# Optimization experiments

Hardware: AMD Instinct MI355X
Metric: run time of the kernel (lower is better)

Reference implementation:

```python
import jax, jax.numpy as jnp
import numpy as np

B, C, H, W = 4, 256, 32, 32
DS, DC, EXP, NSL, NH = 16, 4, 2, 16, 2
DI = EXP * C
DTR = (C + 15) // 16


def layer_norm(x, w, b, eps=1e-5):
    m = x.mean(-1, keepdims=True)
    v = ((x - m) ** 2).mean(-1, keepdims=True)
    return (x - m) / jnp.sqrt(v + eps) * w + b


def conv2d(x, w, b, groups=1, pad=1):
    y = jax.lax.conv_general_dilated(x, w, (1, 1), [(pad, pad), (pad, pad)],
        dimension_numbers=('NCHW', 'OIHW', 'NCHW'), feature_group_count=groups)
    return y + b[None, :, None, None]


def causal_conv1d(x, w, b):
    k = w.shape[-1]
    y = jax.lax.conv_general_dilated(x, w, (1,), [(k - 1, 0)],
        dimension_numbers=('NCH', 'OIH', 'NCH'), feature_group_count=x.shape[1])
    return y + b[None, :, None]


def selective_scan(u, delta, A, Bm, Cm, D, z):
    # u, delta, z: (b,d,l); A: (d,n); Bm, Cm: (b,n,l); D: (d,)
    dA = jnp.exp(jnp.einsum('bdl,dn->lbdn', delta, A))
    dBu = jnp.einsum('bdl,bnl->lbdn', delta * u, Bm)
    Cl = jnp.moveaxis(Cm, -1, 0)  # (l,b,n)
    def step(s, inp):
        dA_t, dBu_t, C_t = inp
        s = dA_t * s + dBu_t
        return s, jnp.einsum('bdn,bn->bd', s, C_t)
    s0 = jnp.zeros(dA.shape[1:], dA.dtype)
    _, ys = jax.lax.scan(step, s0, (dA, dBu, Cl))
    y = jnp.moveaxis(ys, 0, -1) + D[None, :, None] * u
    return y * jax.nn.silu(z)


def mamba_inner(xz, cw, cb, xpw, dtw, dtb, A, D):
    d = xz.shape[1] // 2
    xm, z = xz[:, :d], xz[:, d:]
    xm = jax.nn.silu(causal_conv1d(xm, cw, cb))
    x_dbl = jnp.einsum('bdl,ed->ble', xm, xpw)  # e = dt_rank + 2*d_state
    dt = x_dbl[..., :DTR]
    Bm = x_dbl[..., DTR:DTR + DS]
    Cm = x_dbl[..., DTR + DS:]
    dt = jax.nn.softplus(jnp.einsum('blr,dr->bdl', dt, dtw) + dtb[None, :, None])
    return selective_scan(xm, dt, A, jnp.moveaxis(Bm, -1, 1), jnp.moveaxis(Cm, -1, 1), D, z)


def mamba_v3(hs, in_w, cw, cb, cbw, cbb, csw, csb, xpw, xpbw, xpsw,
             dtw, dtb, dtbw, dtbb, dtsw, dtsb, Alog, Ablog, Aslog, D, Db, Ds, outw):
    b, l, dm = hs.shape
    xz = jnp.einsum('bld,ed->bel', hs, in_w)  # (b, 2*DI, l)
    A, A_b, A_s = -jnp.exp(Alog), -jnp.exp(Ablog), -jnp.exp(Aslog)
    out = mamba_inner(xz, cw, cb, xpw, dtw, dtb, A, D)
    out_b = mamba_inner(xz[:, :, ::-1], cbw, cbb, xpbw, dtbw, dtbb, A_b, Db)
    # slice scan: torch.chunk(nslices,-1) -> stack(-1) -> flatten(-2)
    xz_s = xz.reshape(b, 2 * DI, NSL, l // NSL).transpose(0, 1, 3, 2).reshape(b, 2 * DI, l)
    out_s = mamba_inner(xz_s, csw, csb, xpsw, dtsw, dtsb, A_s, Ds)
    # restore: reshape(b,d,nslices,l//nslices).permute(0,1,3,2).flatten(-2)
    out_s = out_s.reshape(b, DI, NSL, l // NSL).transpose(0, 1, 3, 2).reshape(b, DI, l)
    comb = out + out_b[:, :, ::-1] + out_s
    return jnp.einsum('bdl,od->blo', comb, outw)


def forward(x, proj1_w, proj1_b, proj2_w, proj2_b, norm_w, norm_b,
            q_w, q_b, k_w, k_b, v_w, v_b, o_w, o_b, fc1_w, fc1_b, dw_w, dw_b,
            in_w, cw, cb, cbw, cbb, csw, csb, xpw, xpbw, xpsw,
            dtw, dtb, dtbw, dtbb, dtsw, dtsb, Alog, Ablog, Aslog, D, Db, Ds, outw):
    b, c, h, w = x.shape
    n = h * w
    x_skip = x
    # torch: x.transpose(1,2).reshape(B,C,H,W) -- memory reinterpret, replicated
    x_flat = jnp.transpose(x, (0, 2, 1, 3)).reshape(b, c, h, w)
    xc = conv2d(x_flat, proj1_w, proj1_b)
    xc = jnp.transpose(xc.reshape(b, c, n), (0, 2, 1))
    xc = layer_norm(xc, norm_w, norm_b)
    dh = c // NH
    Q = (xc @ q_w.T + q_b).reshape(b, n, NH, dh).transpose(0, 2, 1, 3)
    K = (xc @ k_w.T + k_b).reshape(b, n, NH, dh).transpose(0, 2, 1, 3)
    V = (xc @ v_w.T + v_b).reshape(b, n, NH, dh).transpose(0, 2, 1, 3)
    scores = jnp.einsum('bhqd,bhkd->bhqk', Q, K) / jnp.sqrt(jnp.float32(dh))
    probs = jax.nn.softmax(scores, axis=-1)
    att = jnp.einsum('bhqk,bhkd->bhqd', probs, V).transpose(0, 2, 1, 3).reshape(b, n, c)
    att = att @ o_w.T + o_b
    # torch: .view(B,C,HW).transpose(1,2) -- memory reinterpret, replicated
    x_att = jnp.transpose(att.reshape(b, c, n), (0, 2, 1))
    xm = mamba_v3(x_att, in_w, cw, cb, cbw, cbb, csw, csb, xpw, xpbw, xpsw,
                  dtw, dtb, dtbw, dtbb, dtsw, dtsb, Alog, Ablog, Aslog, D, Db, Ds, outw)
    xm = jnp.transpose(xm, (0, 2, 1)).reshape(b, c, h, w)
    xm = jax.nn.relu(conv2d(xm, proj1_w, proj1_b))  # proj1 reused (as in source)
    xm = jax.nn.relu(conv2d(xm, proj2_w, proj2_b, pad=0))
    xs = jnp.transpose(xm.reshape(b, c, n), (0, 2, 1))
    xf = xs @ fc1_w.T + fc1_b
    xd = jnp.transpose(xf, (0, 2, 1)).reshape(b, c, h, w)
    xd = conv2d(xd, dw_w, dw_b, groups=c)
    xd = jnp.transpose(xd.reshape(b, c, n), (0, 2, 1))
    out = jnp.transpose(xd.reshape(b, h, w, c), (0, 3, 1, 2)) + x_skip
    return out


def setup_inputs():
    keys = iter(jax.random.split(jax.random.key(0), 64))
    def rn(shape, s=0.02):
        return jax.random.normal(next(keys), shape, jnp.float32) * s
    Alog = jnp.log(jnp.tile(jnp.arange(1, DS + 1, dtype=jnp.float32), (DI, 1)))
    return dict(
        x=jax.random.normal(next(keys), (B, C, H, W), jnp.float32),
        proj1_w=rn((C, C, 3, 3)), proj1_b=jnp.zeros((C,), jnp.float32),
        proj2_w=rn((C, C, 1, 1)), proj2_b=jnp.zeros((C,), jnp.float32),
        norm_w=jnp.ones((C,), jnp.float32), norm_b=jnp.zeros((C,), jnp.float32),
        q_w=rn((C, C)), q_b=jnp.zeros((C,), jnp.float32),
        k_w=rn((C, C)), k_b=jnp.zeros((C,), jnp.float32),
        v_w=rn((C, C)), v_b=jnp.zeros((C,), jnp.float32),
        o_w=rn((C, C)), o_b=jnp.zeros((C,), jnp.float32),
        fc1_w=rn((C, C)), fc1_b=jnp.zeros((C,), jnp.float32),
        dw_w=rn((C, 1, 3, 3)), dw_b=jnp.zeros((C,), jnp.float32),
        in_w=rn((2 * DI, C)),
        cw=rn((DI, 1, DC), 0.1), cb=jnp.zeros((DI,), jnp.float32),
        cbw=rn((DI, 1, DC), 0.1), cbb=jnp.zeros((DI,), jnp.float32),
        csw=rn((DI, 1, DC), 0.1), csb=jnp.zeros((DI,), jnp.float32),
        xpw=rn((DTR + 2 * DS, DI)), xpbw=rn((DTR + 2 * DS, DI)), xpsw=rn((DTR + 2 * DS, DI)),
        dtw=rn((DI, DTR), 0.1), dtb=jnp.full((DI,), -4.6, jnp.float32),
        dtbw=rn((DI, DTR), 0.1), dtbb=jnp.full((DI,), -4.6, jnp.float32),
        dtsw=rn((DI, DTR), 0.1), dtsb=jnp.full((DI,), -4.6, jnp.float32),
        Alog=Alog, Ablog=Alog, Aslog=Alog,
        D=jnp.ones((DI,), jnp.float32), Db=jnp.ones((DI,), jnp.float32), Ds=jnp.ones((DI,), jnp.float32),
        outw=rn((C, DI)),
    )


def reference(x, proj1_w, proj1_b, proj2_w, proj2_b, norm_w, norm_b,
              q_w, q_b, k_w, k_b, v_w, v_b, o_w, o_b, fc1_w, fc1_b, dw_w, dw_b,
              in_w, cw, cb, cbw, cbb, csw, csb, xpw, xpbw, xpsw,
              dtw, dtb, dtbw, dtbb, dtsw, dtsb, Alog, Ablog, Aslog, D, Db, Ds, outw):
    return forward(x, proj1_w, proj1_b, proj2_w, proj2_b, norm_w, norm_b,
                   q_w, q_b, k_w, k_b, v_w, v_b, o_w, o_b, fc1_w, fc1_b, dw_w, dw_b,
                   in_w, cw, cb, cbw, cbb, csw, csb, xpw, xpbw, xpsw,
                   dtw, dtb, dtbw, dtbb, dtsw, dtsb, Alog, Ablog, Aslog, D, Db, Ds, outw)
```

## Files before the change

### kernel.cpp

```cpp
#include <hip/hip_runtime.h>


#define LOG2E 1.4426950408889634f
#define NCH 16
#define LCH 64

typedef unsigned short u16;
typedef unsigned int u32;
typedef __attribute__((ext_vector_type(8))) short bf16x8;
typedef __attribute__((ext_vector_type(4))) float f32x4;

__device__ __forceinline__ u16 f2b(float f) {
  u32 u = __builtin_bit_cast(u32, f);
  u32 r = (u + 0x7fffu + ((u >> 16) & 1u)) >> 16;
  return (u16)r;
}
__device__ __forceinline__ float b2f(u16 h) {
  u32 u = ((u32)h) << 16;
  return __builtin_bit_cast(float, u);
}

#define DPP_ADD(p, ctrl)                                                   \
  (p) += __builtin_bit_cast(float, __builtin_amdgcn_update_dpp(            \
             0, __builtin_bit_cast(int, (p)), ctrl, 0xF, 0xF, true))

static const long BRS = 44544;

__global__ __launch_bounds__(256) void pack_branch_k(
    float* __restrict__ dst, const float* __restrict__ cw,
    const float* __restrict__ cb, const float* __restrict__ xpw,
    const float* __restrict__ dtw, const float* __restrict__ dtb,
    const float* __restrict__ Alog, const float* __restrict__ Dv) {
  int t = blockIdx.x * 256 + threadIdx.x;
  if (t < 2048) dst[t] = cw[t];
  else if (t < 2560) dst[t] = cb[t - 2048];
  else if (t < 27136) dst[t] = xpw[t - 2560];
  else if (t < 35328) dst[t] = dtw[t - 27136];
  else if (t < 35840) dst[t] = dtb[t - 35328];
  else if (t < 44032) dst[t] = -expf(Alog[t - 35840]) * LOG2E;
  else if (t < 44544) dst[t] = Dv[t - 44032];
}

__global__ __launch_bounds__(256) void pack_wb_k(
    const float* __restrict__ qw, const float* __restrict__ kw,
    const float* __restrict__ vw, const float* __restrict__ ow,
    const float* __restrict__ inw, const float* __restrict__ outw,
    const float* __restrict__ p2w, const float* __restrict__ fc1w,
    const float* __restrict__ qb, const float* __restrict__ kb,
    const float* __restrict__ vb, u16* __restrict__ WB,
    float* __restrict__ QBIAS) {
  int t = blockIdx.x * 256 + threadIdx.x;
  if (t < 65536) WB[t] = f2b(qw[t]);
  else if (t < 131072) WB[t] = f2b(kw[t - 65536]);
  else if (t < 196608) WB[t] = f2b(vw[t - 131072]);
  else if (t < 262144) WB[t] = f2b(ow[t - 196608]);
  else if (t < 524288) WB[t] = f2b(inw[t - 262144]);
  else if (t < 655360) WB[t] = f2b(outw[t - 524288]);
  else if (t < 720896) WB[t] = f2b(p2w[t - 655360]);
  else if (t < 786432) WB[t] = f2b(fc1w[t - 720896]);
  else if (t < 787200) {
    int i = t - 786432;
    QBIAS[i] = (i < 256) ? qb[i] : (i < 512 ? kb[i - 256] : vb[i - 512]);
  }
}

__global__ __launch_bounds__(256) void pack_wc_k(const float* __restrict__ w,
                                                 u16* __restrict__ wc) {
  int t = blockIdx.x * 256 + threadIdx.x;
  int ci = t & 255, khw = (t >> 8) % 9, co = t / 2304;
  wc[t] = f2b(w[co * 2304 + ci * 9 + khw]);
}

__global__ __launch_bounds__(256) void xin_k(const float* __restrict__ x,
                                             u16* __restrict__ xin) {
  int t = blockIdx.x * 256 + threadIdx.x;
  int ci = t & 255, w = (t >> 8) & 31, h = (t >> 13) & 31, b = t >> 18;
  int idx = ci * 32 + h;
  xin[t] = f2b(x[((long)b << 18) + ((long)(idx & 255) << 10) +
                 ((idx >> 8) << 5) + w]);
}

__global__ __launch_bounds__(256, 2) void conv_mfma_k(
    const u16* __restrict__ in, const u16* __restrict__ wc,
    const float* __restrict__ bias, float* __restrict__ outF,
    u16* __restrict__ outH, int relu) {
  __shared__ u16 ldsA[4][64][8];
  __shared__ u16 ldsB[4][64][8];
  int m0 = blockIdx.x * 64, n0 = blockIdx.y * 64;
  int tid = threadIdx.x;
  int lane = tid & 63, wv = tid >> 6;
  int row = tid & 63, k8 = tid >> 6;
  int l = m0 + row;
  int h = (l >> 5) & 31, w = l & 31;
  int rlo = lane & 15, khl = lane >> 4;
  f32x4 acc[4];
  #pragma unroll
  for (int n = 0; n < 4; ++n) acc[n] = (f32x4){0.f, 0.f, 0.f, 0.f};
  for (int t = 0; t < 72; ++t) {
    int kh = t / 24, r = t % 24, kw = r >> 3, ci0 = (r & 7) << 5;
    __syncthreads();
    bf16x8 av = (bf16x8){0, 0, 0, 0, 0, 0, 0, 0};
    int hh = h + kh - 1, ww = w + kw - 1;
    if ((unsigned)hh < 32u && (unsigned)ww < 32u)
      av = *(const bf16x8*)&in[(long)(l + (kh - 1) * 32 + (kw - 1)) * 256 +
                               ci0 + k8 * 8];
    *(bf16x8*)&ldsA[k8][row][0] = av;
    *(bf16x8*)&ldsB[k8][row][0] =
        *(const bf16x8*)&wc[(long)(n0 + row) * 2304 + t * 32 + k8 * 8];
    __syncthreads();
    bf16x8 af = *(const bf16x8*)&ldsA[khl][wv * 16 + rlo][0];
    #pragma unroll
    for (int n = 0; n < 4; ++n) {
      bf16x8 bf = *(const bf16x8*)&ldsB[khl][n * 16 + rlo][0];
      acc[n] = __builtin_amdgcn_mfma_f32_16x16x32_bf16(af, bf, acc[n], 0, 0, 0);
    }
  }
  int rowb = (lane >> 4) * 4;
  #pragma unroll
  for (int n = 0; n < 4; ++n) {
    int gn = n0 + n * 16 + rlo;
    float bv = bias[gn];
    #pragma unroll
    for (int j = 0; j < 4; ++j) {
      int gm = m0 + wv * 16 + rowb + j;
      float v = acc[n][j] + bv;
      if (relu) v = fmaxf(v, 0.f);
      long oi = (long)gm * 256 + gn;
      if (outH) outH[oi] = f2b(v);
      else outF[oi] = v;
    }
  }
}

__global__ __launch_bounds__(256) void layernorm_k(const float* __restrict__ x,
                                                   const float* __restrict__ w,
                                                   const float* __restrict__ b,
                                                   u16* __restrict__ o) {
  int row = blockIdx.x * 4 + (threadIdx.x >> 6);
  int lane = threadIdx.x & 63;
  float4 v = ((const float4*)(x + (long)row * 256))[lane];
  float s = v.x + v.y + v.z + v.w;
  #pragma unroll
  for (int m = 32; m; m >>= 1) s += __shfl_xor(s, m);
  float mean = s * (1.f / 256.f);
  float4 dv = {v.x - mean, v.y - mean, v.z - mean, v.w - mean};
  float vs = dv.x * dv.x + dv.y * dv.y + dv.z * dv.z + dv.w * dv.w;
  #pragma unroll
  for (int m = 32; m; m >>= 1) vs += __shfl_xor(vs, m);
  float inv = rsqrtf(vs * (1.f / 256.f) + 1e-5f);
  float4 wv = ((const float4*)w)[lane];
  float4 bv = ((const float4*)b)[lane];
  u32 lo = (u32)f2b(dv.x * inv * wv.x + bv.x) |
           ((u32)f2b(dv.y * inv * wv.y + bv.y) << 16);
  u32 hi = (u32)f2b(dv.z * inv * wv.z + bv.z) |
           ((u32)f2b(dv.w * inv * wv.w + bv.w) << 16);
  ((uint2*)(o + (long)row * 256))[lane] = make_uint2(lo, hi);
}

__global__ __launch_bounds__(256) void softmax_k(const float* __restrict__ S,
                                                 u16* __restrict__ P) {
  int row = blockIdx.x * 4 + (threadIdx.x >> 6);
  int lane = threadIdx.x & 63;
  const float4* p = (const float4*)(S + (long)row * 1024);
  float4 v[4];
  float m = -1e30f;
  #pragma unroll
  for (int i = 0; i < 4; ++i) {
    v[i] = p[lane * 4 + i];
    m = fmaxf(m, fmaxf(fmaxf(v[i].x, v[i].y), fmaxf(v[i].z, v[i].w)));
  }
  #pragma unroll
  for (int q = 32; q; q >>= 1) m = fmaxf(m, __shfl_xor(m, q));
  float s = 0.f;
  #pragma unroll
  for (int i = 0; i < 4; ++i) {
    v[i].x = expf(v[i].x - m); v[i].y = expf(v[i].y - m);
    v[i].z = expf(v[i].z - m); v[i].w = expf(v[i].w - m);
    s += v[i].x + v[i].y + v[i].z + v[i].w;
  }
  #pragma unroll
  for (int q = 32; q; q >>= 1) s += __shfl_xor(s, q);
  float inv = 1.f / s;
  uint2* q2 = (uint2*)(P + (long)row * 1024);
  #pragma unroll
  for (int i = 0; i < 4; ++i) {
    u32 lo = (u32)f2b(v[i].x * inv) | ((u32)f2b(v[i].y * inv) << 16);
    u32 hi = (u32)f2b(v[i].z * inv) | ((u32)f2b(v[i].w * inv) << 16);
    q2[lane * 4 + i] = make_uint2(lo, hi);
  }
}

__global__ __launch_bounds__(256, 2) void bgemm_k(
    const u16* __restrict__ A, const u16* __restrict__ B,
    const float* __restrict__ bias, float* __restrict__ OutF,
    u16* __restrict__ OutH, int M, int N, int K,
    int lda, int ldb, int ldo, int zdiv,
    long a_zb, long a_zh, long b_zb, long b_zh, long o_zb, long o_zh,
    float alpha, int act) {
  __shared__ u16 ldsA[4][128][8];
  __shared__ u16 ldsB[4][128][8];
  int z = blockIdx.z, zb = z / zdiv, zh = z - zb * zdiv;
  const u16* Ab = A + zb * a_zb + zh * a_zh;
  const u16* Bb = B + zb * b_zb + zh * b_zh;
  long ob = zb * o_zb + zh * o_zh;
  int m0 = blockIdx.x * 128, n0 = blockIdx.y * 128;
  int tid = threadIdx.x;
  int lane = tid & 63, wv = tid >> 6;
  int wr = wv >> 1, wc = wv & 1;
  int r1 = tid & 127, h1 = tid >> 7;
  int r2 = r1, h2 = h1 + 2;
  const u16* a1 = Ab + (long)(m0 + r1) * lda + h1 * 8;
  const u16* a2 = Ab + (long)(m0 + r2) * lda + h2 * 8;
  const u16* b1 = Bb + (long)(n0 + r1) * ldb + h1 * 8;
  const u16* b2 = Bb + (long)(n0 + r2) * ldb + h2 * 8;

  f32x4 acc[4][4];
  #pragma unroll
  for (int i = 0; i < 4; ++i)
    #pragma unroll
    for (int j = 0; j < 4; ++j) acc[i][j] = (f32x4){0.f, 0.f, 0.f, 0.f};

  bf16x8 ra1 = *(const bf16x8*)a1;
  bf16x8 ra2 = *(const bf16x8*)a2;
  bf16x8 rb1 = *(const bf16x8*)b1;
  bf16x8 rb2 = *(const bf16x8*)b2;

  int nt = K >> 5;
  int kh = lane >> 4, rlo = lane & 15;
  for (int t = 0; t < nt; ++t) {
    __syncthreads();
    *(bf16x8*)&ldsA[h1][r1][0] = ra1;
    *(bf16x8*)&ldsA[h2][r2][0] = ra2;
    *(bf16x8*)&ldsB[h1][r1][0] = rb1;
    *(bf16x8*)&ldsB[h2][r2][0] = rb2;
    if (t + 1 < nt) {
      int ko = (t + 1) << 5;
      ra1 = *(const bf16x8*)(a1 + ko);
      ra2 = *(const bf16x8*)(a2 + ko);
      rb1 = *(const bf16x8*)(b1 + ko);
      rb2 = *(const bf16x8*)(b2 + ko);
    }
    __syncthreads();
    bf16x8 af[4], bfr[4];
    #pragma unroll
    for (int m = 0; m < 4; ++m)
      af[m] = *(const bf16x8*)&ldsA[kh][wr * 64 + m * 16 + rlo][0];
    #pragma unroll
    for (int n = 0; n < 4; ++n)
      bfr[n] = *(const bf16x8*)&ldsB[kh][wc * 64 + n * 16 + rlo][0];
    #pragma unroll
    for (int m = 0; m < 4; ++m)
      #pragma unroll
      for (int n = 0; n < 4; ++n)
        acc[m][n] = __builtin_amdgcn_mfma_f32_16x16x32_bf16(af[m], bfr[n],
                                                            acc[m][n], 0, 0, 0);
  }
  int rowb = (lane >> 4) * 4;
  #pragma unroll
  for (int m = 0; m < 4; ++m) {
    #pragma unroll
    for (int n = 0; n < 4; ++n) {
      int gn = n0 + wc * 64 + n * 16 + rlo;
      float bv = bias ? bias[gn] : 0.f;
      #pragma unroll
      for (int j = 0; j < 4; ++j) {
        int gm = m0 + wr * 64 + m * 16 + rowb + j;
        float v = acc[m][n][j] * alpha + bv;
        if (act == 1) v = fmaxf(v, 0.f);
        long oi = ob + (long)gm * ldo + gn;
        if (OutH) OutH[oi] = f2b(v);
        else OutF[oi] = v;
      }
    }
  }
}

__global__ __launch_bounds__(256) void vt_k(const u16* __restrict__ qkv,
                                            u16* __restrict__ vt) {
  int t = blockIdx.x * 256 + threadIdx.x;
  int j = t & 1023, d = (t >> 10) & 127, bh = t >> 17;
  int b = bh >> 1, h = bh & 1;
  vt[t] = qkv[((long)(b * 1024 + j)) * 768 + 512 + h * 128 + d];
}

__global__ __launch_bounds__(256) void xatt_k(const float* __restrict__ hs,
                                              u16* __restrict__ xa) {
  int t = blockIdx.x * 256 + threadIdx.x;
  int dm = t & 255, l = (t >> 8) & 1023, b = t >> 18;
  xa[t] = f2b(hs[((long)b << 18) + dm * 1024 + l]);
}

__device__ __forceinline__ int brmap(int br, int j) {
  if (br == 0) return j;
  if (br == 1) return 1023 - j;
  return ((j & 15) << 6) | (j >> 4);
}

__global__ __launch_bounds__(256) void cconv_k(const float* __restrict__ xz,
                                               const float* __restrict__ pk,
                                               float* __restrict__ xmc,
                                               u16* __restrict__ zs) {
  long t = (long)blockIdx.x * 256 + threadIdx.x;
  int d = (int)(t & 511);
  long r = t >> 9;
  int j = (int)(r & 1023);
  int bb = (int)(r >> 10);
  int b = bb & 3, br = bb >> 2;
  const float* pb = pk + (long)br * BRS;
  float acc = pb[2048 + d];
  #pragma unroll
  for (int tap = 0; tap < 4; ++tap) {
    int jj = j - 3 + tap;
    if (jj >= 0) {
      int l = brmap(br, jj);
      acc = fmaf(xz[(((long)b << 10) + l) * 1024 + d], pb[d * 4 + tap], acc);
    }
  }
  float sig = 1.f / (1.f + expf(-acc));
  xmc[t] = acc * sig;
  int l = brmap(br, j);
  float zv = xz[(((long)b << 10) + l) * 1024 + 512 + d];
  zs[t] = f2b(zv / (1.f + expf(-zv)));
}

__global__ __launch_bounds__(256) void gemm_k(
    const float* __restrict__ A, const float* __restrict__ B,
    const float* __restrict__ bias, float* __restrict__ Out,
    int M, int N, int K,
    int a_sm, int a_sk, int b_sn, int b_sk, int o_sm,
    int zdiv, long a_zb, long a_zh, long b_zb, long b_zh, long o_zb, long o_zh,
    long bias_zb, float alpha, int act, const float* __restrict__ Aux) {
  int z = blockIdx.z, zb = z / zdiv, zh = z % zdiv;
  const float* Ab = A + zb * a_zb + zh * a_zh;
  const float* Bb = B + zb * b_zb + zh * b_zh;
  const float* biasb = bias ? (bias + zb * bias_zb) : nullptr;
  long oo = zb * o_zb + zh * o_zh;
  __shared__ float As[16][68];
  __shared__ float Bs[16][68];
  int m0 = blockIdx.x * 64, n0 = blockIdx.y * 64;
  int tid = threadIdx.x;
  int tm = tid >> 4, tn = tid & 15;
  float acc[4][4] = {};
  for (int k0 = 0; k0 < K; k0 += 16) {
    #pragma unroll
    for (int it = 0; it < 4; ++it) {
      int i = tid + it * 256;
      if (a_sk == 1) {
        int rr = i >> 4, kk = i & 15;
        int gm = m0 + rr, gk = k0 + kk;
        float av = 0.f;
        if (gm < M && gk < K) av = Ab[(long)gm * a_sm + gk];
        As[kk][rr] = av;
      } else {
        int rr = i & 63, kk = i >> 6;
        int gm = m0 + rr, gk = k0 + kk;
        float av = 0.f;
        if (gm < M && gk < K) av = Ab[(long)gm * a_sm + (long)gk * a_sk];
        As[kk][rr] = av;
      }
      if (b_sk == 1) {
        int rr = i >> 4, kk = i & 15;
        int gn = n0 + rr, gk = k0 + kk;
        float bv = 0.f;
        if (gn < N && gk < K) bv = Bb[(long)gn * b_sn + gk];
        Bs[kk][rr] = bv;
      } else {
        int rr = i & 63, kk = i >> 6;
        int gn = n0 + rr, gk = k0 + kk;
        float bv = 0.f;
        if (gn < N && gk < K) bv = Bb[(long)gn * b_sn + (long)gk * b_sk];
        Bs[kk][rr] = bv;
      }
    }
    __syncthreads();
    #pragma unroll
    for (int kk = 0; kk < 16; ++kk) {
      float ar[4], br_[4];
      #pragma unroll
      for (int q = 0; q < 4; ++q) ar[q] = As[kk][tm * 4 + q];
      #pragma unroll
      for (int q = 0; q < 4; ++q) br_[q] = Bs[kk][tn * 4 + q];
      #pragma unroll
      for (int qi = 0; qi < 4; ++qi)
        #pragma unroll
        for (int qj = 0; qj < 4; ++qj)
          acc[qi][qj] = fmaf(ar[qi], br_[qj], acc[qi][qj]);
    }
    __syncthreads();
  }
  #pragma unroll
  for (int qi = 0; qi < 4; ++qi) {
    int gm = m0 + tm * 4 + qi;
    if (gm >= M) continue;
    #pragma unroll
    for (int qj = 0; qj < 4; ++qj) {
      int gn = n0 + tn * 4 + qj;
      if (gn >= N) continue;
      float v = acc[qi][qj] * alpha + (biasb ? biasb[gn] : 0.f);
      long oid = oo + (long)gm * o_sm + gn;
      if (act == 3) {
        float sp = (v > 30.f) ? v : log1pf(expf(v));
        ((float2*)Out)[oid] = make_float2(sp, Aux[oid]);
      } else {
        if (act == 1) v = fmaxf(v, 0.f);
        else if (act == 2) v = (v > 30.f) ? v : log1pf(expf(v));
        Out[oid] = v;
      }
    }
  }
}


__global__ __launch_bounds__(256) void scanA_k(
    const float2* __restrict__ du, const float* __restrict__ xdbl,
    const float* __restrict__ pk, float* __restrict__ SE,
    float* __restrict__ PC) {
  __shared__ float bs[LCH][16];
  int tid = threadIdx.x;
  int wv = tid >> 6, lane = tid & 63;
  int q = lane & 3, dl = lane >> 2;
  int bb = blockIdx.x >> 3, dch = blockIdx.x & 7;
  int br = bb >> 2, b = bb & 3;
  int d = dch * 64 + wv * 16 + dl;
  int c = blockIdx.y;
  long xdb = (long)br * 196608 + (long)b * 49152 + (long)(c * LCH) * 48;
  {
    int j = tid >> 2, g = tid & 3;
    *(float4*)&bs[j][g * 4] = *(const float4*)&xdbl[xdb + j * 48 + 16 + g * 4];
  }
  __syncthreads();
  const float* pb = pk + (long)br * BRS;
  float4 Aln = *(const float4*)&pb[35840 + d * 16 + q * 4];
  long obase = ((long)bb << 19) + (long)(c * LCH) * 512 + d;
  const float2* pdu = du + obase;
  float4 s = {0.f, 0.f, 0.f, 0.f};
  float S = 0.f;
  #pragma unroll 4
  for (int jl = 0; jl < LCH; ++jl) {
    float2 dv = pdu[(long)jl * 512];
    float w = dv.x * dv.y;
    float4 Bv = *(const float4*)&bs[jl][q * 4];
    s.x = fmaf(exp2f(dv.x * Aln.x), s.x, w * Bv.x);
    s.y = fmaf(exp2f(dv.x * Aln.y), s.y, w * Bv.y);
    s.z = fmaf(exp2f(dv.x * Aln.z), s.z, w * Bv.z);
    s.w = fmaf(exp2f(dv.x * Aln.w), s.w, w * Bv.w);
    S += dv.x;
  }
  long si = ((((long)bb) * NCH + c) * 512 + d) * 16 + q * 4;
  *(float4*)&SE[si] = s;
  float4 P = {exp2f(Aln.x * S), exp2f(Aln.y * S),
              exp2f(Aln.z * S), exp2f(Aln.w * S)};
  *(float4*)&PC[si] = P;
}

__global__ __launch_bounds__(256) void scanB_k(const float* __restrict__ SE,
                                               const float* __restrict__ PC,
                                               float* __restrict__ SI) {
  long t = (long)blockIdx.x * 256 + threadIdx.x;
  int n = (int)(t & 15);
  int d = (int)((t >> 4) & 511);
  int bb = (int)(t >> 13);
  float run = 0.f;
  for (int c = 0; c < NCH; ++c) {
    long si = (((long)bb * NCH + c) * 512 + d) * 16 + n;
    SI[si] = run;
    run = fmaf(PC[si], run, SE[si]);
  }
}

__global__ __launch_bounds__(256) void scanC_k(
    const float2* __restrict__ du, const float* __restrict__ xdbl,
    const u16* __restrict__ zs, const float* __restrict__ pk,
    const float* __restrict__ SI, u16* __restrict__ y) {
  __shared__ float bcs[LCH][32];
  int tid = threadIdx.x;
  int wv = tid >> 6, lane = tid & 63;
  int q = lane & 3, dl = lane >> 2;
  int bb = blockIdx.x >> 3, dch = blockIdx.x & 7;
  int br = bb >> 2, b = bb & 3;
  int d = dch * 64 + wv * 16 + dl;
  int c = blockIdx.y;
  long xdb = (long)br * 196608 + (long)b * 49152 + (long)(c * LCH) * 48;
  #pragma unroll
  for (int i = 0; i < 2; ++i) {
    int idx = tid + i * 256;
    int j = idx >> 3, g = idx & 7;
    *(float4*)&bcs[j][g * 4] = *(const float4*)&xdbl[xdb + j * 48 + 16 + g * 4];
  }
  __syncthreads();
  const float* pb = pk + (long)br * BRS;
  float4 Aln = *(const float4*)&pb[35840 + d * 16 + q * 4];
  float Dv = pb[44032 + d];
  long obase = ((long)bb << 19) + (long)(c * LCH) * 512 + d;
  long si = ((((long)bb) * NCH + c) * 512 + d) * 16 + q * 4;
  float4 s = *(const float4*)&SI[si];
  const float2* pdu = du + obase;
  const u16* pzs = zs + obase;
  u16* py = y + obase;
  #pragma unroll 4
  for (int jl = 0; jl < LCH; ++jl) {
    float2 dv = pdu[(long)jl * 512];
    float w = dv.x * dv.y;
    float4 Bv = *(const float4*)&bcs[jl][q * 4];
    float4 Cv = *(const float4*)&bcs[jl][16 + q * 4];
    s.x = fmaf(exp2f(dv.x * Aln.x), s.x, w * Bv.x);
    s.y = fmaf(exp2f(dv.x * Aln.y), s.y, w * Bv.y);
    s.z = fmaf(exp2f(dv.x * Aln.z), s.z, w * Bv.z);
    s.w = fmaf(exp2f(dv.x * Aln.w), s.w, w * Bv.w);
    float p = s.x * Cv.x;
    p = fmaf(s.y, Cv.y, p);
    p = fmaf(s.z, Cv.z, p);
    p = fmaf(s.w, Cv.w, p);
    DPP_ADD(p, 0xB1);
    DPP_ADD(p, 0x4E);
    if (q == 0)
      py[(long)jl * 512] = f2b((p + Dv * dv.y) * b2f(pzs[(long)jl * 512]));
  }
}

__global__ __launch_bounds__(256) void combine_k(const u16* __restrict__ y,
                                                 u16* __restrict__ comb) {
  long t = (long)blockIdx.x * 256 + threadIdx.x;
  int d = (int)(t & 511);
  long r = t >> 9;
  int l = (int)(r & 1023);
  int b = (int)(r >> 10);
  int j2 = ((l & 63) << 4) | (l >> 6);
  float v = b2f(y[(((long)b << 10) + l) * 512 + d])
          + b2f(y[(((long)(4 + b) << 10) + (1023 - l)) * 512 + d])
          + b2f(y[(((long)(8 + b) << 10) + j2) * 512 + d]);
  comb[t] = f2b(v);
}

__global__ __launch_bounds__(256) void dw_k(const float* __restrict__ xf,
                                            const float* __restrict__ dww,
                                            const float* __restrict__ dwb,
                                            const float* __restrict__ x,
                                            float* __restrict__ out) {
  int t = blockIdx.x;
  int b = t >> 5, h = t & 31;
  int c = threadIdx.x;
  float wv[9];
  #pragma unroll
  for (int k = 0; k < 9; ++k) wv[k] = dww[c * 9 + k];
  float bb = dwb[c];
  for (int w = 0; w < 32; ++w) {
    float acc = bb;
    #pragma unroll
    for (int kh = 0; kh < 3; ++kh) {
      int hh = h + kh - 1;
      if ((unsigned)hh >= 32u) continue;
      #pragma unroll
      for (int kw = 0; kw < 3; ++kw) {
        int ww = w + kw - 1;
        if ((unsigned)ww >= 32u) continue;
        acc = fmaf(xf[(((long)b << 10) + (hh << 5) + ww) * 256 + c],
                   wv[kh * 3 + kw], acc);
      }
    }
    long oi = (((long)b * 256 + c) * 32 + h) * 32 + w;
    out[oi] = acc + x[oi];
  }
}

extern "C" void kernel_launch(void* const* d_in, const int* in_sizes, int n_in,
                              void* d_out, int out_size, void* d_ws, size_t ws_size,
                              hipStream_t stream) {
  (void)in_sizes; (void)n_in; (void)out_size; (void)ws_size;
  const float* x    = (const float*)d_in[0];
  const float* p1w  = (const float*)d_in[1];
  const float* p1b  = (const float*)d_in[2];
  const float* p2w  = (const float*)d_in[3];
  const float* p2b  = (const float*)d_in[4];
  const float* nw   = (const float*)d_in[5];
  const float* nb   = (const float*)d_in[6];
  const float* qw   = (const float*)d_in[7];
  const float* qb   = (const float*)d_in[8];
  const float* kw   = (const float*)d_in[9];
  const float* kb   = (const float*)d_in[10];
  const float* vw   = (const float*)d_in[11];
  const float* vb   = (const float*)d_in[12];
  const float* ow   = (const float*)d_in[13];
  const float* ob   = (const float*)d_in[14];
  const float* fc1w = (const float*)d_in[15];
  const float* fc1b = (const float*)d_in[16];
  const float* dww  = (const float*)d_in[17];
  const float* dwb  = (const float*)d_in[18];
  const float* inw  = (const float*)d_in[19];
  const float* cw   = (const float*)d_in[20];
  const float* cb   = (const float*)d_in[21];
  const float* cbw  = (const float*)d_in[22];
  const float* cbb  = (const float*)d_in[23];
  const float* csw  = (const float*)d_in[24];
  const float* csb  = (const float*)d_in[25];
  const float* xpw  = (const float*)d_in[26];
  const float* xpbw = (const float*)d_in[27];
  const float* xpsw = (const float*)d_in[28];
  const float* dtw  = (const float*)d_in[29];
  const float* dtb  = (const float*)d_in[30];
  const float* dtbw = (const float*)d_in[31];
  const float* dtbb = (const float*)d_in[32];
  const float* dtsw = (const float*)d_in[33];
  const float* dtsb = (const float*)d_in[34];
  const float* Alog = (const float*)d_in[35];
  const float* Ablog= (const float*)d_in[36];
  const float* Aslog= (const float*)d_in[37];
  const float* Dv   = (const float*)d_in[38];
  const float* Dbv  = (const float*)d_in[39];
  const float* Dsv  = (const float*)d_in[40];
  const float* outw = (const float*)d_in[41];
  float* out = (float*)d_out;

  float* ws    = (float*)d_ws;
  float* PB    = ws;
  u16*   WCONV = (u16*)(ws + 140000);
  u16*   WB    = (u16*)(ws + 440000);
  float* QBIAS = ws + 840000;
  u16*   XINB  = (u16*)(ws + 850000);
  float* R     = ws + 1400000;
  float*  XZ   = R;
  float2* DU   = (float2*)R;
  float*  XMC  = R + 12700000;
  u16*    Y    = (u16*)(R + 12700000);
  float*  SE   = R + 14300000;
  float*  PC   = R + 15900000;
  float*  SI   = R + 17500000;
  u16*   COMBB = (u16*)(R + 17500000);
  u16*    ZS   = (u16*)(R + 19100000);
  float*  XDBL = R + 25400000;
  float* XCT   = R + 4300000;
  u16*   XCTB  = (u16*)(R + 5400000);
  u16*   QKVB  = (u16*)(R + 6000000);
  u16*   VT    = (u16*)(R + 7600000);
  float* SC    = R + 8200000;
  u16*   P     = (u16*)(R + 16600000);
  u16*   ATTB  = (u16*)(R + 18800000);
  float* HS    = R + 19400000;
  u16*   XATTB = (u16*)(R + 20500000);
  u16*   XMBB  = (u16*)R;
  u16*   XM2B  = (u16*)(R + 600000);
  u16*   XPB   = (u16*)(R + 1200000);
  float* XF    = R + 1800000;

  u16* WQKVB = WB;
  u16* OWB   = WB + 196608;
  u16* INWB  = WB + 262144;
  u16* OUTWB = WB + 524288;
  u16* P2WB  = WB + 655360;
  u16* FC1WB = WB + 720896;

  auto bgemm = [&](const u16* A, const u16* Bm, const float* bias,
                   float* OutF, u16* OutH, int M, int N, int K,
                   int lda, int ldb, int ldo, int nz, int zdiv,
                   long a_zb, long a_zh, long b_zb, long b_zh,
                   long o_zb, long o_zh, float alpha, int act) {
    dim3 g(M / 128, N / 128, nz);
    bgemm_k<<<g, 256, 0, stream>>>(A, Bm, bias, OutF, OutH, M, N, K,
                                   lda, ldb, ldo, zdiv, a_zb, a_zh,
                                   b_zb, b_zh, o_zb, o_zh, alpha, act);
  };

  pack_branch_k<<<174, 256, 0, stream>>>(PB, cw, cb, xpw, dtw, dtb, Alog, Dv);
  pack_branch_k<<<174, 256, 0, stream>>>(PB + BRS, cbw, cbb, xpbw, dtbw, dtbb, Ablog, Dbv);
  pack_branch_k<<<174, 256, 0, stream>>>(PB + 2 * BRS, csw, csb, xpsw, dtsw, dtsb, Aslog, Dsv);
  pack_wb_k<<<3075, 256, 0, stream>>>(qw, kw, vw, ow, inw, outw, p2w, fc1w,
                                      qb, kb, vb, WB, QBIAS);
  pack_wc_k<<<2304, 256, 0, stream>>>(p1w, WCONV);
  xin_k<<<4096, 256, 0, stream>>>(x, XINB);

  conv_mfma_k<<<dim3(64, 4), 256, 0, stream>>>(XINB, WCONV, p1b, XCT, nullptr, 0);
  layernorm_k<<<1024, 256, 0, stream>>>(XCT, nw, nb, XCTB);

  bgemm(XCTB, WQKVB, QBIAS, nullptr, QKVB, 4096, 768, 256, 256, 256, 768,
        1, 1, 0, 0, 0, 0, 0, 0, 1.f, 0);
  vt_k<<<4096, 256, 0, stream>>>(QKVB, VT);

  bgemm(QKVB, QKVB + 256, nullptr, SC, nullptr, 1024, 1024, 128, 768, 768, 1024,
        8, 2, 786432, 128, 786432, 128, 2097152, 1048576,
        0.08838834764831845f, 0);
  softmax_k<<<2048, 256, 0, stream>>>(SC, P);

  bgemm(P, VT, nullptr, nullptr, ATTB, 1024, 128, 1024, 1024, 1024, 256,
        8, 2, 2097152, 1048576, 262144, 131072, 262144, 128, 1.f, 0);

  bgemm(ATTB, OWB, ob, HS, nullptr, 4096, 256, 256, 256, 256, 256,
        1, 1, 0, 0, 0, 0, 0, 0, 1.f, 0);
  xatt_k<<<4096, 256, 0, stream>>>(HS, XATTB);

  bgemm(XATTB, INWB, nullptr, XZ, nullptr, 1024, 1024, 256, 256, 256, 1024,
        4, 1, 262144, 0, 0, 0, 1048576, 0, 1.f, 0);

  cconv_k<<<24576, 256, 0, stream>>>(XZ, PB, XMC, ZS);

  {
    dim3 g(64, 1, 3);
    gemm_k<<<g, 256, 0, stream>>>(XMC, PB + 2560, nullptr, XDBL, 4096, 48, 512,
                                  512, 1, 512, 1, 48, 1, 2097152, 0, BRS, 0,
                                  196608, 0, 0, 1.f, 0, nullptr);
  }
  {
    dim3 g(64, 8, 3);
    gemm_k<<<g, 256, 0, stream>>>(XDBL, PB + 27136, PB + 35328, (float*)DU,
                                  4096, 512, 16, 48, 1, 16, 1, 512, 1,
                                  196608, 0, BRS, 0, 2097152, 0, BRS,
                                  1.f, 3, XMC);
  }

  scanA_k<<<dim3(96, NCH), 256, 0, stream>>>(DU, XDBL, PB, SE, PC);
  scanB_k<<<384, 256, 0, stream>>>(SE, PC, SI);
  scanC_k<<<dim3(96, NCH), 256, 0, stream>>>(DU, XDBL, ZS, PB, SI, Y);

  combine_k<<<8192, 256, 0, stream>>>(Y, COMBB);

  bgemm(COMBB, OUTWB, nullptr, nullptr, XMBB, 4096, 256, 512, 512, 512, 256,
        1, 1, 0, 0, 0, 0, 0, 0, 1.f, 0);

  conv_mfma_k<<<dim3(64, 4), 256, 0, stream>>>(XMBB, WCONV, p1b, nullptr, XM2B, 1);

  bgemm(XM2B, P2WB, p2b, nullptr, XPB, 4096, 256, 256, 256, 256, 256,
        1, 1, 0, 0, 0, 0, 0, 0, 1.f, 1);

  bgemm(XPB, FC1WB, fc1b, XF, nullptr, 4096, 256, 256, 256, 256, 256,
        1, 1, 0, 0, 0, 0, 0, 0, 1.f, 0);

  dw_k<<<128, 256, 0, stream>>>(XF, dww, dwb, x, out);
}
```

Before: 659.1 us.

## Fold dt projection into x_proj weights and run fused bf16 MFMA GEMM

Precomposes dt_proj with the dt rows of x_proj into one weight matrix, so a single bf16 MFMA GEMM (N=640, padded) produces B/C and the softplus delta directly. This replaces the two fp32 scalar gemm_k launches, with a new epilogue mode that writes B/C to a compact buffer and packs delta with u. The in_proj and fc1 outputs become bf16, which halves their traffic. dw_k is rewritten to stage each channel plane in LDS with coalesced output writes, and the three branch-pack launches are merged into one. The cost is lower precision for the delta path and the xz and fc1 intermediates, plus extra weight-packing kernels and wasted padded columns in the fused GEMM.

Measured after the change: 672.0 us. About the same (+2.0%).

```diff
diff --git a/kernel.cpp b/kernel.cpp
--- a/kernel.cpp
+++ b/kernel.cpp
@@ -26,19 +26,21 @@
 
 static const long BRS = 44544;
 
-__global__ __launch_bounds__(256) void pack_branch_k(
-    float* __restrict__ dst, const float* __restrict__ cw,
-    const float* __restrict__ cb, const float* __restrict__ xpw,
-    const float* __restrict__ dtw, const float* __restrict__ dtb,
-    const float* __restrict__ Alog, const float* __restrict__ Dv) {
+struct BrP { const float *cw, *cb, *xpw, *dtw, *dtb, *Al, *Dv; };
+
+__global__ __launch_bounds__(256) void pack_branch_k(float* __restrict__ dst0,
+                                                     BrP p0, BrP p1, BrP p2) {
+  int z = blockIdx.y;
+  BrP p = (z == 0) ? p0 : ((z == 1) ? p1 : p2);
+  float* dst = dst0 + (long)z * BRS;
   int t = blockIdx.x * 256 + threadIdx.x;
-  if (t < 2048) dst[t] = cw[t];
-  else if (t < 2560) dst[t] = cb[t - 2048];
-  else if (t < 27136) dst[t] = xpw[t - 2560];
-  else if (t < 35328) dst[t] = dtw[t - 27136];
-  else if (t < 35840) dst[t] = dtb[t - 35328];
-  else if (t < 44032) dst[t] = -expf(Alog[t - 35840]) * LOG2E;
-  else if (t < 44544) dst[t] = Dv[t - 44032];
+  if (t < 2048) dst[t] = p.cw[t];
+  else if (t < 2560) dst[t] = p.cb[t - 2048];
+  else if (t < 27136) dst[t] = p.xpw[t - 2560];
+  else if (t < 35328) dst[t] = p.dtw[t - 27136];
+  else if (t < 35840) dst[t] = p.dtb[t - 35328];
+  else if (t < 44032) dst[t] = -expf(p.Al[t - 35840]) * LOG2E;
+  else if (t < 44544) dst[t] = p.Dv[t - 44032];
 }
 
 __global__ __launch_bounds__(256) void pack_wb_k(
@@ -80,6 +82,44 @@
                  ((idx >> 8) << 5) + w]);
 }
 
+__global__ __launch_bounds__(256) void pack_wmb_k(const float* __restrict__ PB,
+                                                  u16* __restrict__ WMB,
+                                                  float* __restrict__ BIA) {
+  int z = blockIdx.y;
+  int t = blockIdx.x * 256 + threadIdx.x;
+  const float* pb = PB + (long)z * BRS;
+  if (t < 16384) {
+    int r = t >> 9, k = t & 511;
+    WMB[((long)z * 640 + r) * 512 + k] = f2b(pb[2560 + (16 + r) * 512 + k]);
+  } else if (t < 65536) {
+    int i = t - 16384;
+    int r = 544 + (i >> 9), k = i & 511;
+    WMB[((long)z * 640 + r) * 512 + k] = 0;
+  } else if (t < 66176) {
+    int i = t - 65536;
+    float v = 0.f;
+    if (i >= 32 && i < 544) v = pb[35328 + (i - 32)];
+    BIA[(long)z * 640 + i] = v;
+  }
+}
+
+__global__ __launch_bounds__(256) void pack_wdt_k(const float* __restrict__ PB,
+                                                  u16* __restrict__ WMB) {
+  int z = blockIdx.y, d = blockIdx.x;
+  const float* pb = PB + (long)z * BRS;
+  float dtwv[16];
+  #pragma unroll
+  for (int r = 0; r < 16; ++r) dtwv[r] = pb[27136 + d * 16 + r];
+  #pragma unroll
+  for (int i = 0; i < 2; ++i) {
+    int k = threadIdx.x + i * 256;
+    float acc = 0.f;
+    #pragma unroll
+    for (int r = 0; r < 16; ++r) acc = fmaf(dtwv[r], pb[2560 + r * 512 + k], acc);
+    WMB[((long)z * 640 + 32 + d) * 512 + k] = f2b(acc);
+  }
+}
+
 __global__ __launch_bounds__(256, 2) void conv_mfma_k(
     const u16* __restrict__ in, const u16* __restrict__ wc,
     const float* __restrict__ bias, float* __restrict__ outF,
@@ -196,12 +236,14 @@
     u16* __restrict__ OutH, int M, int N, int K,
     int lda, int ldb, int ldo, int zdiv,
     long a_zb, long a_zh, long b_zb, long b_zh, long o_zb, long o_zh,
-    float alpha, int act) {
+    float alpha, int act, int bias_zb, float* __restrict__ Out2,
+    const float* __restrict__ Aux) {
   __shared__ u16 ldsA[4][128][8];
   __shared__ u16 ldsB[4][128][8];
   int z = blockIdx.z, zb = z / zdiv, zh = z - zb * zdiv;
   const u16* Ab = A + zb * a_zb + zh * a_zh;
   const u16* Bb = B + zb * b_zb + zh * b_zh;
+  const float* biasb = bias ? bias + (long)zb * bias_zb : nullptr;
   long ob = zb * o_zb + zh * o_zh;
   int m0 = blockIdx.x * 128, n0 = blockIdx.y * 128;
   int tid = threadIdx.x;
@@ -261,15 +303,25 @@
     #pragma unroll
     for (int n = 0; n < 4; ++n) {
       int gn = n0 + wc * 64 + n * 16 + rlo;
-      float bv = bias ? bias[gn] : 0.f;
+      float bv = biasb ? biasb[gn] : 0.f;
       #pragma unroll
       for (int j = 0; j < 4; ++j) {
         int gm = m0 + wr * 64 + m * 16 + rowb + j;
         float v = acc[m][n][j] * alpha + bv;
-        if (act == 1) v = fmaxf(v, 0.f);
-        long oi = ob + (long)gm * ldo + gn;
-        if (OutH) OutH[oi] = f2b(v);
-        else OutF[oi] = v;
+        if (act == 4) {
+          if (gn < 32) {
+            Out2[(long)(zb * 4096 + gm) * 32 + gn] = v;
+          } else if (gn < 544) {
+            float sp = (v > 30.f) ? v : log1pf(expf(v));
+            long di = (long)(zb * 4096 + gm) * 512 + (gn - 32);
+            ((float2*)OutF)[di] = make_float2(sp, Aux[di]);
+          }
+        } else {
+          if (act == 1) v = fmaxf(v, 0.f);
+          long oi = ob + (long)gm * ldo + gn;
+          if (OutH) OutH[oi] = f2b(v);
+          else OutF[oi] = v;
+        }
       }
     }
   }
@@ -296,9 +348,10 @@
   return ((j & 15) << 6) | (j >> 4);
 }
 
-__global__ __launch_bounds__(256) void cconv_k(const float* __restrict__ xz,
+__global__ __launch_bounds__(256) void cconv_k(const u16* __restrict__ xzb,
                                                const float* __restrict__ pk,
                                                float* __restrict__ xmc,
+                                               u16* __restrict__ xmcb,
                                                u16* __restrict__ zs) {
   long t = (long)blockIdx.x * 256 + threadIdx.x;
   int d = (int)(t & 511);
@@ -313,103 +366,18 @@
     int jj = j - 3 + tap;
     if (jj >= 0) {
       int l = brmap(br, jj);
-      acc = fmaf(xz[(((long)b << 10) + l) * 1024 + d], pb[d * 4 + tap], acc);
+      acc = fmaf(b2f(xzb[(((long)b << 10) + l) * 1024 + d]), pb[d * 4 + tap],
+                 acc);
     }
   }
   float sig = 1.f / (1.f + expf(-acc));
-  xmc[t] = acc * sig;
+  float u = acc * sig;
+  xmc[t] = u;
+  xmcb[t] = f2b(u);
   int l = brmap(br, j);
-  float zv = xz[(((long)b << 10) + l) * 1024 + 512 + d];
+  float zv = b2f(xzb[(((long)b << 10) + l) * 1024 + 512 + d]);
   zs[t] = f2b(zv / (1.f + expf(-zv)));
 }
-
-__global__ __launch_bounds__(256) void gemm_k(
-    const float* __restrict__ A, const float* __restrict__ B,
-    const float* __restrict__ bias, float* __restrict__ Out,
-    int M, int N, int K,
-    int a_sm, int a_sk, int b_sn, int b_sk, int o_sm,
-    int zdiv, long a_zb, long a_zh, long b_zb, long b_zh, long o_zb, long o_zh,
-    long bias_zb, float alpha, int act, const float* __restrict__ Aux) {
-  int z = blockIdx.z, zb = z / zdiv, zh = z % zdiv;
-  const float* Ab = A + zb * a_zb + zh * a_zh;
-  const float* Bb = B + zb * b_zb + zh * b_zh;
-  const float* biasb = bias ? (bias + zb * bias_zb) : nullptr;
-  long oo = zb * o_zb + zh * o_zh;
-  __shared__ float As[16][68];
-  __shared__ float Bs[16][68];
-  int m0 = blockIdx.x * 64, n0 = blockIdx.y * 64;
-  int tid = threadIdx.x;
-  int tm = tid >> 4, tn = tid & 15;
-  float acc[4][4] = {};
-  for (int k0 = 0; k0 < K; k0 += 16) {
-    #pragma unroll
-    for (int it = 0; it < 4; ++it) {
-      int i = tid + it * 256;
-      if (a_sk == 1) {
-        int rr = i >> 4, kk = i & 15;
-        int gm = m0 + rr, gk = k0 + kk;
-        float av = 0.f;
-        if (gm < M && gk < K) av = Ab[(long)gm * a_sm + gk];
-        As[kk][rr] = av;
-      } else {
-        int rr = i & 63, kk = i >> 6;
-        int gm = m0 + rr, gk = k0 + kk;
-        float av = 0.f;
-        if (gm < M && gk < K) av = Ab[(long)gm * a_sm + (long)gk * a_sk];
-        As[kk][rr] = av;
-      }
-      if (b_sk == 1) {
-        int rr = i >> 4, kk = i & 15;
-        int gn = n0 + rr, gk = k0 + kk;
-        float bv = 0.f;
-        if (gn < N && gk < K) bv = Bb[(long)gn * b_sn + gk];
-        Bs[kk][rr] = bv;
-      } else {
-        int rr = i & 63, kk = i >> 6;
-        int gn = n0 + rr, gk = k0 + kk;
-        float bv = 0.f;
-        if (gn < N && gk < K) bv = Bb[(long)gn * b_sn + (long)gk * b_sk];
-        Bs[kk][rr] = bv;
-      }
-    }
-    __syncthreads();
-    #pragma unroll
-    for (int kk = 0; kk < 16; ++kk) {
-      float ar[4], br_[4];
-      #pragma unroll
-      for (int q = 0; q < 4; ++q) ar[q] = As[kk][tm * 4 + q];
-      #pragma unroll
-      for (int q = 0; q < 4; ++q) br_[q] = Bs[kk][tn * 4 + q];
-      #pragma unroll
-      for (int qi = 0; qi < 4; ++qi)
-        #pragma unroll
-        for (int qj = 0; qj < 4; ++qj)
-          acc[qi][qj] = fmaf(ar[qi], br_[qj], acc[qi][qj]);
-    }
-    __syncthreads();
-  }
-  #pragma unroll
-  for (int qi = 0; qi < 4; ++qi) {
-    int gm = m0 + tm * 4 + qi;
-    if (gm >= M) continue;
-    #pragma unroll
-    for (int qj = 0; qj < 4; ++qj) {
-      int gn = n0 + tn * 4 + qj;
-      if (gn >= N) continue;
-      float v = acc[qi][qj] * alpha + (biasb ? biasb[gn] : 0.f);
-      long oid = oo + (long)gm * o_sm + gn;
-      if (act == 3) {
-        float sp = (v > 30.f) ? v : log1pf(expf(v));
-        ((float2*)Out)[oid] = make_float2(sp, Aux[oid]);
-      } else {
-        if (act == 1) v = fmaxf(v, 0.f);
-        else if (act == 2) v = (v > 30.f) ? v : log1pf(expf(v));
-        Out[oid] = v;
-      }
-    }
-  }
-}
-
 
 __global__ __launch_bounds__(256) void scanA_k(
     const float2* __restrict__ du, const float* __restrict__ xdbl,
@@ -423,10 +391,10 @@
   int br = bb >> 2, b = bb & 3;
   int d = dch * 64 + wv * 16 + dl;
   int c = blockIdx.y;
-  long xdb = (long)br * 196608 + (long)b * 49152 + (long)(c * LCH) * 48;
+  long xdb = (long)br * 131072 + (long)b * 32768 + (long)(c * LCH) * 32;
   {
     int j = tid >> 2, g = tid & 3;
-    *(float4*)&bs[j][g * 4] = *(const float4*)&xdbl[xdb + j * 48 + 16 + g * 4];
+    *(float4*)&bs[j][g * 4] = *(const float4*)&xdbl[xdb + j * 32 + g * 4];
   }
   __syncthreads();
   const float* pb = pk + (long)br * BRS;
@@ -480,12 +448,12 @@
   int br = bb >> 2, b = bb & 3;
   int d = dch * 64 + wv * 16 + dl;
   int c = blockIdx.y;
-  long xdb = (long)br * 196608 + (long)b * 49152 + (long)(c * LCH) * 48;
+  long xdb = (long)br * 131072 + (long)b * 32768 + (long)(c * LCH) * 32;
   #pragma unroll
   for (int i = 0; i < 2; ++i) {
     int idx = tid + i * 256;
     int j = idx >> 3, g = idx & 7;
-    *(float4*)&bcs[j][g * 4] = *(const float4*)&xdbl[xdb + j * 48 + 16 + g * 4];
+    *(float4*)&bcs[j][g * 4] = *(const float4*)&xdbl[xdb + j * 32 + g * 4];
   }
   __syncthreads();
   const float* pb = pk + (long)br * BRS;
@@ -532,19 +500,30 @@
   comb[t] = f2b(v);
 }
 
-__global__ __launch_bounds__(256) void dw_k(const float* __restrict__ xf,
+__global__ __launch_bounds__(256) void dw_k(const u16* __restrict__ xfb,
                                             const float* __restrict__ dww,
                                             const float* __restrict__ dwb,
                                             const float* __restrict__ x,
                                             float* __restrict__ out) {
-  int t = blockIdx.x;
-  int b = t >> 5, h = t & 31;
-  int c = threadIdx.x;
+  __shared__ float plane[1024];
+  int bc = blockIdx.x;
+  int b = bc >> 8, c = bc & 255;
+  int tid = threadIdx.x;
+  #pragma unroll
+  for (int i = 0; i < 4; ++i) {
+    int n = tid + i * 256;
+    plane[n] = b2f(xfb[(((long)b << 10) + n) * 256 + c]);
+  }
+  __syncthreads();
   float wv[9];
   #pragma unroll
   for (int k = 0; k < 9; ++k) wv[k] = dww[c * 9 + k];
   float bb = dwb[c];
-  for (int w = 0; w < 32; ++w) {
+  long obase = ((long)(b * 256 + c)) << 10;
+  #pragma unroll
+  for (int i = 0; i < 4; ++i) {
+    int n = tid + i * 256;
+    int h = n >> 5, w = n & 31;
     float acc = bb;
     #pragma unroll
     for (int kh = 0; kh < 3; ++kh) {
@@ -554,12 +533,10 @@
       for (int kw = 0; kw < 3; ++kw) {
         int ww = w + kw - 1;
         if ((unsigned)ww >= 32u) continue;
-        acc = fmaf(xf[(((long)b << 10) + (hh << 5) + ww) * 256 + c],
-                   wv[kh * 3 + kw], acc);
+        acc = fmaf(plane[hh * 32 + ww], wv[kh * 3 + kw], acc);
       }
     }
-    long oi = (((long)b * 256 + c) * 32 + h) * 32 + w;
-    out[oi] = acc + x[oi];
+    out[obase + n] = acc + x[obase + n];
   }
 }
 
@@ -618,29 +595,33 @@
   float* QBIAS = ws + 840000;
   u16*   XINB  = (u16*)(ws + 850000);
   float* R     = ws + 1400000;
-  float*  XZ   = R;
+
+  u16*    XZB  = (u16*)R;
   float2* DU   = (float2*)R;
-  float*  XMC  = R + 12700000;
-  u16*    Y    = (u16*)(R + 12700000);
-  float*  SE   = R + 14300000;
-  float*  PC   = R + 15900000;
-  float*  SI   = R + 17500000;
-  u16*   COMBB = (u16*)(R + 17500000);
-  u16*    ZS   = (u16*)(R + 19100000);
-  float*  XDBL = R + 25400000;
+  u16*    ZS   = (u16*)(R + 12600000);
+  float*  XMC  = R + 15750000;
+  float*  SE   = R + 15750000;
+  float*  PC   = R + 17350000;
+  float*  SI   = R + 19000000;
+  u16*    Y    = (u16*)(R + 20600000);
+  u16*    XMCB = (u16*)(R + 22050000);
+  u16*   COMBB = (u16*)(R + 23750000);
+  float*  XDBL = R + 25200000;
+  u16*    WMB  = (u16*)(R + 25600000);
+  float*  BIA  = R + 26100000;
   float* XCT   = R + 4300000;
   u16*   XCTB  = (u16*)(R + 5400000);
   u16*   QKVB  = (u16*)(R + 6000000);
   u16*   VT    = (u16*)(R + 7600000);
   float* SC    = R + 8200000;
   u16*   P     = (u16*)(R + 16600000);
-  u16*   ATTB  = (u16*)(R + 18800000);
-  float* HS    = R + 19400000;
-  u16*   XATTB = (u16*)(R + 20500000);
+  u16*   ATTB  = (u16*)(R + 20900000);
+  float* HS    = R + 21500000;
+  u16*   XATTB = (u16*)(R + 22600000);
   u16*   XMBB  = (u16*)R;
   u16*   XM2B  = (u16*)(R + 600000);
   u16*   XPB   = (u16*)(R + 1200000);
-  float* XF    = R + 1800000;
+  u16*   XFB   = (u16*)(R + 1800000);
 
   u16* WQKVB = WB;
   u16* OWB   = WB + 196608;
@@ -653,58 +634,53 @@
                    float* OutF, u16* OutH, int M, int N, int K,
                    int lda, int ldb, int ldo, int nz, int zdiv,
                    long a_zb, long a_zh, long b_zb, long b_zh,
-                   long o_zb, long o_zh, float alpha, int act) {
+                   long o_zb, long o_zh, float alpha, int act,
+                   int bias_zb, float* Out2, const float* Aux) {
     dim3 g(M / 128, N / 128, nz);
     bgemm_k<<<g, 256, 0, stream>>>(A, Bm, bias, OutF, OutH, M, N, K,
                                    lda, ldb, ldo, zdiv, a_zb, a_zh,
-                                   b_zb, b_zh, o_zb, o_zh, alpha, act);
+                                   b_zb, b_zh, o_zb, o_zh, alpha, act,
+                                   bias_zb, Out2, Aux);
   };
 
-  pack_branch_k<<<174, 256, 0, stream>>>(PB, cw, cb, xpw, dtw, dtb, Alog, Dv);
-  pack_branch_k<<<174, 256, 0, stream>>>(PB + BRS, cbw, cbb, xpbw, dtbw, dtbb, Ablog, Dbv);
-  pack_branch_k<<<174, 256, 0, stream>>>(PB + 2 * BRS, csw, csb, xpsw, dtsw, dtsb, Aslog, Dsv);
+  BrP b0 = {cw, cb, xpw, dtw, dtb, Alog, Dv};
+  BrP b1 = {cbw, cbb, xpbw, dtbw, dtbb, Ablog, Dbv};
+  BrP b2 = {csw, csb, xpsw, dtsw, dtsb, Aslog, Dsv};
+  pack_branch_k<<<dim3(174, 3), 256, 0, stream>>>(PB, b0, b1, b2);
   pack_wb_k<<<3075, 256, 0, stream>>>(qw, kw, vw, ow, inw, outw, p2w, fc1w,
                                       qb, kb, vb, WB, QBIAS);
   pack_wc_k<<<2304, 256, 0, stream>>>(p1w, WCONV);
   xin_k<<<4096, 256, 0, stream>>>(x, XINB);
+  pack_wmb_k<<<dim3(259, 3), 256, 0, stream>>>(PB, WMB, BIA);
+  pack_wdt_k<<<dim3(512, 3), 256, 0, stream>>>(PB, WMB);
 
   conv_mfma_k<<<dim3(64, 4), 256, 0, stream>>>(XINB, WCONV, p1b, XCT, nullptr, 0);
   layernorm_k<<<1024, 256, 0, stream>>>(XCT, nw, nb, XCTB);
 
   bgemm(XCTB, WQKVB, QBIAS, nullptr, QKVB, 4096, 768, 256, 256, 256, 768,
-        1, 1, 0, 0, 0, 0, 0, 0, 1.f, 0);
+        1, 1, 0, 0, 0, 0, 0, 0, 1.f, 0, 0, nullptr, nullptr);
   vt_k<<<4096, 256, 0, stream>>>(QKVB, VT);
 
   bgemm(QKVB, QKVB + 256, nullptr, SC, nullptr, 1024, 1024, 128, 768, 768, 1024,
         8, 2, 786432, 128, 786432, 128, 2097152, 1048576,
-        0.08838834764831845f, 0);
+        0.08838834764831845f, 0, 0, nullptr, nullptr);
   softmax_k<<<2048, 256, 0, stream>>>(SC, P);
 
   bgemm(P, VT, nullptr, nullptr, ATTB, 1024, 128, 1024, 1024, 1024, 256,
-        8, 2, 2097152, 1048576, 262144, 131072, 262144, 128, 1.f, 0);
+        8, 2, 2097152, 1048576, 262144, 131072, 262144, 128, 1.f, 0,
+        0, nullptr, nullptr);
 
   bgemm(ATTB, OWB, ob, HS, nullptr, 4096, 256, 256, 256, 256, 256,
-        1, 1, 0, 0, 0, 0, 0, 0, 1.f, 0);
+        1, 1, 0, 0, 0, 0, 0, 0, 1.f, 0, 0, nullptr, nullptr);
   xatt_k<<<4096, 256, 0, stream>>>(HS, XATTB);
 
-  bgemm(XATTB, INWB, nullptr, XZ, nullptr, 1024, 1024, 256, 256, 256, 1024,
-        4, 1, 262144, 0, 0, 0, 1048576, 0, 1.f, 0);
-
-  cconv_k<<<24576, 256, 0, stream>>>(XZ, PB, XMC, ZS);
-
-  {
-    dim3 g(64, 1, 3);
-    gemm_k<<<g, 256, 0, stream>>>(XMC, PB + 2560, nullptr, XDBL, 4096, 48, 512,
-                                  512, 1, 512, 1, 48, 1, 2097152, 0, BRS, 0,
-                                  196608, 0, 0, 1.f, 0, nullptr);
-  }
-  {
-    dim3 g(64, 8, 3);
-    gemm_k<<<g, 256, 0, stream>>>(XDBL, PB + 27136, PB + 35328, (float*)DU,
-                                  4096, 512, 16, 48, 1, 16, 1, 512, 1,
-                                  196608, 0, BRS, 0, 2097152, 0, BRS,
-                                  1.f, 3, XMC);
-  }
+  bgemm(XATTB, INWB, nullptr, nullptr, XZB, 1024, 1024, 256, 256, 256, 1024,
+        4, 1, 262144, 0, 0, 0, 1048576, 0, 1.f, 0, 0, nullptr, nullptr);
+
+  cconv_k<<<24576, 256, 0, stream>>>(XZB, PB, XMC, XMCB, ZS);
+
+  bgemm(XMCB, WMB, BIA, (float*)DU, nullptr, 4096, 640, 512, 512, 512, 0,
+        3, 1, 2097152, 0, 327680, 0, 0, 0, 1.f, 4, 640, XDBL, XMC);
 
   scanA_k<<<dim3(96, NCH), 256, 0, stream>>>(DU, XDBL, PB, SE, PC);
   scanB_k<<<384, 256, 0, stream>>>(SE, PC, SI);
@@ -713,15 +689,15 @@
   combine_k<<<8192, 256, 0, stream>>>(Y, COMBB);
 
   bgemm(COMBB, OUTWB, nullptr, nullptr, XMBB, 4096, 256, 512, 512, 512, 256,
-        1, 1, 0, 0, 0, 0, 0, 0, 1.f, 0);
+        1, 1, 0, 0, 0, 0, 0, 0, 1.f, 0, 0, nullptr, nullptr);
 
   conv_mfma_k<<<dim3(64, 4), 256, 0, stream>>>(XMBB, WCONV, p1b, nullptr, XM2B, 1);
 
   bgemm(XM2B, P2WB, p2b, nullptr, XPB, 4096, 256, 256, 256, 256, 256,
-        1, 1, 0, 0, 0, 0, 0, 0, 1.f, 1);
-
-  bgemm(XPB, FC1WB, fc1b, XF, nullptr, 4096, 256, 256, 256, 256, 256,
-        1, 1, 0, 0, 0, 0, 0, 0, 1.f, 0);
-
-  dw_k<<<128, 256, 0, stream>>>(XF, dww, dwb, x, out);
-}
+        1, 1, 0, 0, 0, 0, 0, 0, 1.f, 1, 0, nullptr, nullptr);
+
+  bgemm(XPB, FC1WB, fc1b, nullptr, XFB, 4096, 256, 256, 256, 256, 256,
+        1, 1, 0, 0, 0, 0, 0, 0, 1.f, 0, 0, nullptr, nullptr);
+
+  dw_k<<<1024, 256, 0, stream>>>(XFB, dww, dwb, x, out);
+}
```
